# Performance work log

Measured on AMD Instinct MI355X. Metric: run time of the kernel, lower is better.

Reference implementation:

```python
import jax, jax.numpy as jnp
import numpy as np

B, T, D = 2, 4096, 512
H, W = 8, 32
HD = D // H            # 64
HIDDEN = 3 * D         # SwiGLU expansion = 3
SCALE = float(np.sqrt(HD))
EPS = 1e-5


def setup_inputs() -> dict:
    key = jax.random.key(0)
    ks = jax.random.split(key, 8)
    s = 0.02  # small init for weight matrices
    return {
        "x": jax.random.normal(ks[0], (B, T, D), dtype=jnp.float32),
        "pre_g": jnp.ones((D,), jnp.float32), "pre_b": jnp.zeros((D,), jnp.float32),
        "wq": jax.random.normal(ks[1], (D, D), jnp.float32) * s,
        "wkv": jax.random.normal(ks[2], (D, 2 * D), jnp.float32) * s,
        "wo": jax.random.normal(ks[3], (D, D), jnp.float32) * s,
        "attn_g": jnp.ones((D,), jnp.float32), "attn_b": jnp.zeros((D,), jnp.float32),
        "freqs": jax.random.normal(ks[4], (D,), jnp.float32) * 0.02,
        "phases": jnp.zeros((D,), jnp.float32),
        "amp": jnp.full((1,), 0.1, jnp.float32),
        "w_gate": jax.random.normal(ks[5], (D, HIDDEN), jnp.float32) * s,
        "w_val": jax.random.normal(ks[6], (D, HIDDEN), jnp.float32) * s,
        "w_proj": jax.random.normal(ks[7], (HIDDEN, D), jnp.float32) * s,
        "ffn_g": jnp.ones((D,), jnp.float32), "ffn_b": jnp.zeros((D,), jnp.float32),
    }


def _ln(x, g, b):
    mu = jnp.mean(x, axis=-1, keepdims=True)
    var = jnp.mean(jnp.square(x - mu), axis=-1, keepdims=True)
    return (x - mu) * jax.lax.rsqrt(var + EPS) * g + b


def _gather_window(z):
    # z: (B, T, H, C) -> nb: (B, T, W, H, C) with nb[:, t, w] = z[:, t-1-w] (zeros if t-1-w < 0)
    zp = jnp.pad(z, ((0, 0), (W, 0), (0, 0), (0, 0)))
    idx = jnp.arange(T)[:, None] + (W - 1) - jnp.arange(W)[None, :]  # (T, W), values in [0, T+W-1)
    return zp[:, idx]  # (B, T, W, H, C)


def reference(x, pre_g, pre_b, wq, wkv, wo, attn_g, attn_b,
              freqs, phases, amp, w_gate, w_val, w_proj, ffn_g, ffn_b):
    h = _ln(x, pre_g, pre_b)

    # ---- multi-head causal tension (sigmoid local attention) ----
    q = (h @ wq).reshape(B, T, H, HD)
    kv = (h @ wkv).reshape(B, T, H, 2 * HD)
    nb_kv = _gather_window(kv)                     # (B, T, W, H, 2*HD)
    nb_k, nb_v = nb_kv[..., :HD], nb_kv[..., HD:]
    tau = jax.nn.sigmoid(jnp.einsum('bthd,btwhd->bthw', q, nb_k) / SCALE)
    msg = jnp.einsum('bthw,btwhd->bthd', tau, nb_v).reshape(B, T, D)
    h = _ln(h + msg @ wo, attn_g, attn_b)

    # ---- oscillatory modulation ----
    pos = jnp.arange(T, dtype=jnp.float32)[:, None]  # (T, 1)
    mod = jnp.sin(pos * freqs + phases)              # (T, D)
    y = h * (1.0 + amp * mod)[None]

    # ---- SwiGLU FFN ----
    z = (jax.nn.silu(y @ w_gate) * (y @ w_val)) @ w_proj
    return _ln(y + z, ffn_g, ffn_b)
```

## Files before the change

### kernel.cpp

```cpp
#include <hip/hip_runtime.h>
#include <hip/hip_bf16.h>
#include <math.h>

#define T_LEN   4096
#define D_DIM   512
#define H_NUM   8
#define HD_DIM  64
#define W_WIN   32
#define HID_DIM 1536
#define M_ROWS  8192
#define QKV_LD  1536
#define BK 64

typedef __hip_bfloat16 bf16;
typedef __bf16  bf16x8 __attribute__((ext_vector_type(8)));
typedef float   f32x4  __attribute__((ext_vector_type(4)));

#define G_AS __attribute__((address_space(1)))
#define L_AS __attribute__((address_space(3)))

__device__ __forceinline__ float b2f(bf16 x) { return __bfloat162float(x); }
__device__ __forceinline__ bf16  f2b(float x){ return __float2bfloat16(x); }

__device__ __forceinline__ void gload_lds16(const bf16* g, bf16* l) {
  __builtin_amdgcn_global_load_lds((const G_AS unsigned int*)g,
                                   (L_AS unsigned int*)l, 16, 0, 0);
}

__device__ __forceinline__ float rdP(const void* p, int i, bool f32) {
  return f32 ? ((const float*)p)[i] : b2f(((const bf16*)p)[i]);
}

__device__ __forceinline__ float wave_reduce_sum(float v) {
  #pragma unroll
  for (int off = 32; off; off >>= 1) v += __shfl_xor(v, off, 64);
  return v;
}

__device__ __forceinline__ bool detect_f32(const unsigned* __restrict__ x) {
  int lane = threadIdx.x & 63;
  int votes = 0;
  #pragma unroll
  for (int i = 0; i < 4; ++i) {
    unsigned e = (x[lane * 4 + i] >> 7) & 0xffu;
    votes += (e >= 90u && e <= 140u) ? 1 : 0;
  }
  float v = wave_reduce_sum((float)votes);
  return v < 200.f;
}

__device__ __forceinline__ void swizzle_xy(int gx, int& bx, int& by) {
  int lid = blockIdx.x;
  int sub = lid & 7;
  int grp = lid >> 3;
  bx = grp % gx;
  by = (grp / gx) * 8 + sub;
}

__global__ __launch_bounds__(256) void ln_kernel(
    const void* __restrict__ in, const void* __restrict__ g, const void* __restrict__ bb,
    void* __restrict__ out, int mode,
    const void* __restrict__ freqs, const void* __restrict__ phases,
    const void* __restrict__ amp,
    const unsigned* __restrict__ xdet, int in_follows, int out_follows)
{
  bool f32  = detect_f32(xdet);
  bool inF  = f32 && (in_follows != 0);
  bool outF = f32 && (out_follows != 0);

  int wave = threadIdx.x >> 6;
  int lane = threadIdx.x & 63;
  int row  = blockIdx.x * 4 + wave;

  float x[8];
  if (inF) {
    const float* rp = (const float*)in + (size_t)row * D_DIM + lane * 8;
    float4 v0 = *reinterpret_cast<const float4*>(rp);
    float4 v1 = *reinterpret_cast<const float4*>(rp + 4);
    x[0]=v0.x; x[1]=v0.y; x[2]=v0.z; x[3]=v0.w;
    x[4]=v1.x; x[5]=v1.y; x[6]=v1.z; x[7]=v1.w;
  } else {
    bf16x8 v = *reinterpret_cast<const bf16x8*>(
        (const bf16*)in + (size_t)row * D_DIM + lane * 8);
    #pragma unroll
    for (int i = 0; i < 8; ++i) x[i] = (float)v[i];
  }

  float s = 0.f, s2 = 0.f;
  #pragma unroll
  for (int i = 0; i < 8; ++i) { s += x[i]; s2 += x[i]*x[i]; }
  s  = wave_reduce_sum(s);
  s2 = wave_reduce_sum(s2);
  float mu   = s * (1.f / D_DIM);
  float var  = s2 * (1.f / D_DIM) - mu * mu;
  float rstd = rsqrtf(var + 1e-5f);

  int t = row & (T_LEN - 1);
  float ampf = (mode == 1) ? rdP(amp, 0, f32) : 0.f;

  float o[8];
  #pragma unroll
  for (int i = 0; i < 8; ++i) {
    int d = lane * 8 + i;
    float val = (x[i] - mu) * rstd * rdP(g, d, f32) + rdP(bb, d, f32);
    if (mode == 1) {
      float m = sinf(fmaf((float)t, rdP(freqs, d, f32), rdP(phases, d, f32)));
      val *= (1.f + ampf * m);
    }
    o[i] = val;
  }

  if (outF) {
    float* op = (float*)out + (size_t)row * D_DIM + lane * 8;
    *reinterpret_cast<float4*>(op)     = make_float4(o[0], o[1], o[2], o[3]);
    *reinterpret_cast<float4*>(op + 4) = make_float4(o[4], o[5], o[6], o[7]);
  } else {
    bf16x8 ov;
    #pragma unroll
    for (int i = 0; i < 8; ++i) ov[i] = (__bf16)o[i];
    *reinterpret_cast<bf16x8*>((bf16*)out + (size_t)row * D_DIM + lane * 8) = ov;
  }
}

__global__ __launch_bounds__(256) void transpose_all_kernel(
    const void* s0, const void* s1, const void* s2, const void* s3,
    const void* s4, const void* s5,
    bf16* d0, bf16* d1, bf16* d2, bf16* d3, bf16* d4, bf16* d5,
    const unsigned* __restrict__ xdet)
{
  bool f32 = detect_f32(xdet);
  int bid = blockIdx.x;
  const void* src; bf16* dst; int R, C, lid, tiles_x;
  if      (bid < 256)  { src=s0; dst=d0; R=512;  C=512;  lid=bid;      tiles_x=16; }
  else if (bid < 768)  { src=s1; dst=d1; R=512;  C=1024; lid=bid-256;  tiles_x=32; }
  else if (bid < 1024) { src=s2; dst=d2; R=512;  C=512;  lid=bid-768;  tiles_x=16; }
  else if (bid < 1792) { src=s3; dst=d3; R=512;  C=1536; lid=bid-1024; tiles_x=48; }
  else if (bid < 2560) { src=s4; dst=d4; R=512;  C=1536; lid=bid-1792; tiles_x=48; }
  else                 { src=s5; dst=d5; R=1536; C=512;  lid=bid-2560; tiles_x=16; }

  __shared__ bf16 tile[32][33];
  int tx = threadIdx.x & 31;
  int ty = threadIdx.x >> 5;
  int c0 = (lid % tiles_x) * 32;
  int r0 = (lid / tiles_x) * 32;
  #pragma unroll
  for (int j = 0; j < 32; j += 8)
    tile[ty + j][tx] = f2b(rdP(src, (size_t)(r0 + ty + j) * C + c0 + tx, f32));
  __syncthreads();
  #pragma unroll
  for (int j = 0; j < 32; j += 8)
    dst[(size_t)(c0 + ty + j) * R + r0 + tx] = tile[tx][ty + j];
}

template<int BNT>
__global__ __launch_bounds__(256) void gemm_tile_kernel(
    const bf16* __restrict__ A, const bf16* __restrict__ Bt,
    bf16* Cout, const bf16* extra, int N, int K, int lda, int mode, int gx)
{
  constexpr int BJ = BNT / 32;
  __shared__ alignas(16) bf16 As[128 * BK];
  __shared__ alignas(16) bf16 Bs[BNT * BK];

  int bx, by; swizzle_xy(gx, bx, by);
  int mbase = by * 128, nbase = bx * BNT;
  int tid  = threadIdx.x;
  int lane = tid & 63;
  int wid  = tid >> 6;
  int quad = lane >> 4, l16 = lane & 15;
  int wm = (wid >> 1) * 64, wn = (wid & 1) * (BNT / 2);

  int srow = tid >> 3;
  int scol = (tid & 7) ^ (srow & 7);
  const bf16* Ag = A  + (size_t)(mbase + srow) * lda + scol * 8;
  const bf16* Bg = Bt + (size_t)(nbase + srow) * K   + scol * 8;

  f32x4 acc[4][BJ] = {};

  for (int kleft = K / BK; kleft > 0; --kleft) {
    __syncthreads();
    #pragma unroll
    for (int j = 0; j < 4; ++j)
      gload_lds16(Ag + (size_t)(j * 32) * lda, &As[j * 2048 + tid * 8]);
    #pragma unroll
    for (int j = 0; j < BJ; ++j)
      gload_lds16(Bg + (size_t)(j * 32) * K,   &Bs[j * 2048 + tid * 8]);
    Ag += BK; Bg += BK;
    __syncthreads();

    #pragma unroll
    for (int ko = 0; ko < 2; ++ko) {
      bf16x8 a[4], b[BJ];
      int c = ((ko * 4 + quad) ^ (l16 & 7)) * 8;
      #pragma unroll
      for (int i = 0; i < 4; ++i)
        a[i] = *reinterpret_cast<const bf16x8*>(&As[(wm + i * 16 + l16) * BK + c]);
      #pragma unroll
      for (int j = 0; j < BJ; ++j)
        b[j] = *reinterpret_cast<const bf16x8*>(&Bs[(wn + j * 16 + l16) * BK + c]);
      #pragma unroll
      for (int i = 0; i < 4; ++i)
        #pragma unroll
        for (int j = 0; j < BJ; ++j)
          acc[i][j] = __builtin_amdgcn_mfma_f32_16x16x32_bf16(a[i], b[j], acc[i][j], 0, 0, 0);
    }
  }

  #pragma unroll
  for (int i = 0; i < 4; ++i)
    #pragma unroll
    for (int j = 0; j < BJ; ++j)
      #pragma unroll
      for (int r = 0; r < 4; ++r) {
        int row = mbase + wm + i * 16 + quad * 4 + r;
        int col = nbase + wn + j * 16 + l16;
        size_t idx = (size_t)row * N + col;
        float cv = acc[i][j][r];
        if (mode == 1) cv += b2f(extra[idx]);
        Cout[idx] = f2b(cv);
      }
}

__global__ __launch_bounds__(256) void gateval_kernel(
    const bf16* __restrict__ A, const bf16* __restrict__ Btg,
    const bf16* __restrict__ Btv, bf16* __restrict__ Cout,
    int N, int K, int lda, int gx)
{
  __shared__ alignas(16) bf16 As [128 * BK];
  __shared__ alignas(16) bf16 Bgs[ 64 * BK];
  __shared__ alignas(16) bf16 Bvs[ 64 * BK];

  int bx, by; swizzle_xy(gx, bx, by);
  int mbase = by * 128, nbase = bx * 64;
  int tid  = threadIdx.x;
  int lane = tid & 63;
  int wid  = tid >> 6;
  int quad = lane >> 4, l16 = lane & 15;
  int wm = (wid >> 1) * 64, wn = (wid & 1) * 32;

  int srow = tid >> 3;
  int scol = (tid & 7) ^ (srow & 7);
  const bf16* Ag = A   + (size_t)(mbase + srow) * lda + scol * 8;
  const bf16* Gg = Btg + (size_t)(nbase + srow) * K   + scol * 8;
  const bf16* Vg = Btv + (size_t)(nbase + srow) * K   + scol * 8;

  f32x4 accg[4][2] = {};
  f32x4 accv[4][2] = {};

  for (int kleft = K / BK; kleft > 0; --kleft) {
    __syncthreads();
    #pragma unroll
    for (int j = 0; j < 4; ++j)
      gload_lds16(Ag + (size_t)(j * 32) * lda, &As[j * 2048 + tid * 8]);
    #pragma unroll
    for (int j = 0; j < 2; ++j) {
      gload_lds16(Gg + (size_t)(j * 32) * K, &Bgs[j * 2048 + tid * 8]);
      gload_lds16(Vg + (size_t)(j * 32) * K, &Bvs[j * 2048 + tid * 8]);
    }
    Ag += BK; Gg += BK; Vg += BK;
    __syncthreads();

    #pragma unroll
    for (int ko = 0; ko < 2; ++ko) {
      bf16x8 a[4], bg[2], bv[2];
      int c = ((ko * 4 + quad) ^ (l16 & 7)) * 8;
      #pragma unroll
      for (int i = 0; i < 4; ++i)
        a[i]  = *reinterpret_cast<const bf16x8*>(&As [(wm + i * 16 + l16) * BK + c]);
      #pragma unroll
      for (int j = 0; j < 2; ++j) {
        bg[j] = *reinterpret_cast<const bf16x8*>(&Bgs[(wn + j * 16 + l16) * BK + c]);
        bv[j] = *reinterpret_cast<const bf16x8*>(&Bvs[(wn + j * 16 + l16) * BK + c]);
      }
      #pragma unroll
      for (int i = 0; i < 4; ++i)
        #pragma unroll
        for (int j = 0; j < 2; ++j) {
          accg[i][j] = __builtin_amdgcn_mfma_f32_16x16x32_bf16(a[i], bg[j], accg[i][j], 0, 0, 0);
          accv[i][j] = __builtin_amdgcn_mfma_f32_16x16x32_bf16(a[i], bv[j], accv[i][j], 0, 0, 0);
        }
    }
  }

  #pragma unroll
  for (int i = 0; i < 4; ++i)
    #pragma unroll
    for (int j = 0; j < 2; ++j)
      #pragma unroll
      for (int r = 0; r < 4; ++r) {
        int row = mbase + wm + i * 16 + quad * 4 + r;
        int col = nbase + wn + j * 16 + l16;
        float g = accg[i][j][r];
        float v = accv[i][j][r];
        Cout[(size_t)row * N + col] = f2b(g / (1.f + expf(-g)) * v);
      }
}

#define VT_BYTES 9216
#define PL_BYTES 2304
#define ATTN_SET (VT_BYTES + PL_BYTES)
__device__ __forceinline__ int vt_addr(int d, int t) { return d * 144 + t * 2; }

__global__ __launch_bounds__(256) void attn_mfma_kernel(bf16* qkv)
{
  __shared__ alignas(16) char lds_raw[4 * ATTN_SET];
  int lane = threadIdx.x & 63;
  int widx = threadIdx.x >> 6;
  int u    = blockIdx.x * 4 + widx;
  int tile = u >> 3, head = u & 7;
  int rowbase = tile * 16;
  int t0   = rowbase & (T_LEN - 1);
  int l16  = lane & 15, quad = lane >> 4;

  char* wbase = lds_raw + widx * ATTN_SET;
  char* Vl = wbase;
  bf16* Pl = (bf16*)(wbase + VT_BYTES);

  #pragma unroll
  for (int it = 0; it < 6; ++it) {
    int chunk = it * 64 + lane;
    int t  = chunk >> 3;
    int dc = chunk & 7;
    int row = rowbase - 32 + t;
    if (row < 0) row = 0;
    bf16x8 v = *reinterpret_cast<const bf16x8*>(
        qkv + (size_t)row * QKV_LD + 512 + head * 128 + 64 + dc * 8);
    #pragma unroll
    for (int jj = 0; jj < 8; ++jj)
      *(bf16*)(Vl + vt_addr(dc * 8 + jj, t)) = (bf16)(__bf16)v[jj];
  }
  bf16x8 z = {};
  *reinterpret_cast<bf16x8*>(Vl + vt_addr(lane, 48)) = z;
  *reinterpret_cast<bf16x8*>(Vl + vt_addr(lane, 56)) = z;

  bf16x8 aq0, aq1;
  {
    const bf16* qrow = qkv + (size_t)(rowbase + l16) * QKV_LD + head * HD_DIM + quad * 8;
    aq0 = *reinterpret_cast<const bf16x8*>(qrow);
    aq1 = *reinterpret_cast<const bf16x8*>(qrow + 32);
  }

  f32x4 sacc[3] = {};
  #pragma unroll
  for (int jt = 0; jt < 3; ++jt) {
    int tok = rowbase - 32 + jt * 16 + l16;
    if (tok < 0) tok = 0;
    const bf16* krow = qkv + (size_t)tok * QKV_LD + 512 + head * 128 + quad * 8;
    bf16x8 b0 = *reinterpret_cast<const bf16x8*>(krow);
    bf16x8 b1 = *reinterpret_cast<const bf16x8*>(krow + 32);
    sacc[jt] = __builtin_amdgcn_mfma_f32_16x16x32_bf16(aq0, b0, sacc[jt], 0, 0, 0);
    sacc[jt] = __builtin_amdgcn_mfma_f32_16x16x32_bf16(aq1, b1, sacc[jt], 0, 0, 0);
  }

  #pragma unroll
  for (int jt = 0; jt < 3; ++jt) {
    int j = jt * 16 + l16;
    #pragma unroll
    for (int r = 0; r < 4; ++r) {
      int i = quad * 4 + r;
      bool valid = (j >= i) && (j <= i + 31) && (t0 - 32 + j >= 0);
      float tau = valid ? 1.f / (1.f + expf(-sacc[jt][r] * 0.125f)) : 0.f;
      Pl[i * 72 + j] = f2b(tau);
    }
  }
  #pragma unroll
  for (int r = 0; r < 4; ++r) Pl[(quad * 4 + r) * 72 + 48 + l16] = f2b(0.f);

  __syncthreads();

  bf16x8 ap0 = *reinterpret_cast<const bf16x8*>((char*)Pl + l16 * 144 + quad * 16);
  bf16x8 ap1 = *reinterpret_cast<const bf16x8*>((char*)Pl + l16 * 144 + 64 + quad * 16);

  f32x4 macc[4] = {};
  #pragma unroll
  for (int nt = 0; nt < 4; ++nt) {
    int d = nt * 16 + l16;
    bf16x8 bv0 = *reinterpret_cast<const bf16x8*>(Vl + vt_addr(d, quad * 8));
    bf16x8 bv1 = *reinterpret_cast<const bf16x8*>(Vl + vt_addr(d, 32 + quad * 8));
    macc[nt] = __builtin_amdgcn_mfma_f32_16x16x32_bf16(ap0, bv0, macc[nt], 0, 0, 0);
    macc[nt] = __builtin_amdgcn_mfma_f32_16x16x32_bf16(ap1, bv1, macc[nt], 0, 0, 0);
  }

  #pragma unroll
  for (int nt = 0; nt < 4; ++nt)
    #pragma unroll
    for (int r = 0; r < 4; ++r)
      qkv[(size_t)(rowbase + quad * 4 + r) * QKV_LD + head * HD_DIM + nt * 16 + l16] =
          f2b(macc[nt][r]);
}

extern "C" void kernel_launch(void* const* d_in, const int* in_sizes, int n_in,
                              void* d_out, int out_size, void* d_ws, size_t ws_size,
                              hipStream_t stream)
{
  const void* x      = d_in[0];
  const void* pre_g  = d_in[1];
  const void* pre_b  = d_in[2];
  const void* wq     = d_in[3];
  const void* wkv    = d_in[4];
  const void* wo     = d_in[5];
  const void* attn_g = d_in[6];
  const void* attn_b = d_in[7];
  const void* freqs  = d_in[8];
  const void* phases = d_in[9];
  const void* amp    = d_in[10];
  const void* w_gate = d_in[11];
  const void* w_val  = d_in[12];
  const void* w_proj = d_in[13];
  const void* ffn_g  = d_in[14];
  const void* ffn_b  = d_in[15];
  const unsigned* xdet = (const unsigned*)x;

  char* ws = (char*)d_ws;
  bf16* Btqkv = (bf16*)(ws + 512);
  bf16* Bto   = (bf16*)(ws + 1573376);
  bf16* Btg   = (bf16*)(ws + 2097664);
  bf16* Btv   = (bf16*)(ws + 3670528);
  bf16* Btp   = (bf16*)(ws + 5243392);
  bf16* h     = (bf16*)(ws + 6816256);
  bf16* qkvb  = (bf16*)(ws + 15204864);
  bf16* gb    = qkvb;

  transpose_all_kernel<<<3328, 256, 0, stream>>>(
      wq, wkv, wo, w_gate, w_val, w_proj,
      Btqkv, Btqkv + 512 * 512, Bto, Btg, Btv, Btp, xdet);

  ln_kernel<<<2048, 256, 0, stream>>>(x, pre_g, pre_b, h, 0,
                                      nullptr, nullptr, nullptr, xdet, 1, 0);

  gemm_tile_kernel<128><<<768, 256, 0, stream>>>(h, Btqkv, qkvb, nullptr,
                                                 1536, 512, 512, 0, 12);

  attn_mfma_kernel<<<1024, 256, 0, stream>>>(qkvb);

  gemm_tile_kernel<64><<<512, 256, 0, stream>>>(qkvb, Bto, h, h,
                                                512, 512, QKV_LD, 1, 8);

  ln_kernel<<<2048, 256, 0, stream>>>(h, attn_g, attn_b, h, 1,
                                      freqs, phases, amp, xdet, 0, 0);

  gateval_kernel<<<1536, 256, 0, stream>>>(h, Btg, Btv, gb,
                                           1536, 512, 512, 24);

  gemm_tile_kernel<64><<<512, 256, 0, stream>>>(gb, Btp, h, h,
                                                512, 1536, QKV_LD, 1, 8);

  ln_kernel<<<2048, 256, 0, stream>>>(h, ffn_g, ffn_b, d_out, 0,
                                      nullptr, nullptr, nullptr, xdet, 0, 1);
}
```

Before: 298.9 us.

## Double-buffer LDS tiles in GEMM kernels to overlap global loads with MFMA

```diff
diff --git a/kernel.cpp b/kernel.cpp
--- a/kernel.cpp
+++ b/kernel.cpp
@@ -18,6 +18,11 @@
 
 #define G_AS __attribute__((address_space(1)))
 #define L_AS __attribute__((address_space(3)))
+
+#define SBAR()        __builtin_amdgcn_s_barrier()
+#define SCHED_FENCE() __builtin_amdgcn_sched_barrier(0)
+#define WAIT_VM(N)    asm volatile("s_waitcnt vmcnt(" #N ")" ::: "memory")
+#define WAIT_LGKM0()  asm volatile("s_waitcnt lgkmcnt(0)" ::: "memory")
 
 __device__ __forceinline__ float b2f(bf16 x) { return __bfloat162float(x); }
 __device__ __forceinline__ bf16  f2b(float x){ return __float2bfloat16(x); }
@@ -158,8 +163,8 @@
     bf16* Cout, const bf16* extra, int N, int K, int lda, int mode, int gx)
 {
   constexpr int BJ = BNT / 32;
-  __shared__ alignas(16) bf16 As[128 * BK];
-  __shared__ alignas(16) bf16 Bs[BNT * BK];
+  __shared__ alignas(16) bf16 As[2][128 * BK];
+  __shared__ alignas(16) bf16 Bs[2][BNT * BK];
 
   int bx, by; swizzle_xy(gx, bx, by);
   int mbase = by * 128, nbase = bx * BNT;
@@ -175,17 +180,33 @@
   const bf16* Bg = Bt + (size_t)(nbase + srow) * K   + scol * 8;
 
   f32x4 acc[4][BJ] = {};
-
-  for (int kleft = K / BK; kleft > 0; --kleft) {
-    __syncthreads();
-    #pragma unroll
-    for (int j = 0; j < 4; ++j)
-      gload_lds16(Ag + (size_t)(j * 32) * lda, &As[j * 2048 + tid * 8]);
-    #pragma unroll
-    for (int j = 0; j < BJ; ++j)
-      gload_lds16(Bg + (size_t)(j * 32) * K,   &Bs[j * 2048 + tid * 8]);
-    Ag += BK; Bg += BK;
-    __syncthreads();
+  int nk = K / BK;
+
+  #pragma unroll
+  for (int j = 0; j < 4; ++j)
+    gload_lds16(Ag + (size_t)(j * 32) * lda, &As[0][j * 2048 + tid * 8]);
+  #pragma unroll
+  for (int j = 0; j < BJ; ++j)
+    gload_lds16(Bg + (size_t)(j * 32) * K,   &Bs[0][j * 2048 + tid * 8]);
+  Ag += BK; Bg += BK;
+
+  for (int t = 0; t < nk; ++t) {
+    int cur = t & 1;
+    if (t + 1 < nk) {
+      int nxt = cur ^ 1;
+      #pragma unroll
+      for (int j = 0; j < 4; ++j)
+        gload_lds16(Ag + (size_t)(j * 32) * lda, &As[nxt][j * 2048 + tid * 8]);
+      #pragma unroll
+      for (int j = 0; j < BJ; ++j)
+        gload_lds16(Bg + (size_t)(j * 32) * K,   &Bs[nxt][j * 2048 + tid * 8]);
+      Ag += BK; Bg += BK;
+      if constexpr (BNT == 128) { WAIT_VM(8); } else { WAIT_VM(6); }
+    } else {
+      WAIT_VM(0);
+    }
+    SBAR();
+    SCHED_FENCE();
 
     #pragma unroll
     for (int ko = 0; ko < 2; ++ko) {
@@ -193,16 +214,20 @@
       int c = ((ko * 4 + quad) ^ (l16 & 7)) * 8;
       #pragma unroll
       for (int i = 0; i < 4; ++i)
-        a[i] = *reinterpret_cast<const bf16x8*>(&As[(wm + i * 16 + l16) * BK + c]);
+        a[i] = *reinterpret_cast<const bf16x8*>(&As[cur][(wm + i * 16 + l16) * BK + c]);
       #pragma unroll
       for (int j = 0; j < BJ; ++j)
-        b[j] = *reinterpret_cast<const bf16x8*>(&Bs[(wn + j * 16 + l16) * BK + c]);
+        b[j] = *reinterpret_cast<const bf16x8*>(&Bs[cur][(wn + j * 16 + l16) * BK + c]);
       #pragma unroll
       for (int i = 0; i < 4; ++i)
         #pragma unroll
         for (int j = 0; j < BJ; ++j)
           acc[i][j] = __builtin_amdgcn_mfma_f32_16x16x32_bf16(a[i], b[j], acc[i][j], 0, 0, 0);
     }
+
+    WAIT_LGKM0();
+    SBAR();
+    SCHED_FENCE();
   }
 
   #pragma unroll
@@ -225,9 +250,9 @@
     const bf16* __restrict__ Btv, bf16* __restrict__ Cout,
     int N, int K, int lda, int gx)
 {
-  __shared__ alignas(16) bf16 As [128 * BK];
-  __shared__ alignas(16) bf16 Bgs[ 64 * BK];
-  __shared__ alignas(16) bf16 Bvs[ 64 * BK];
+  __shared__ alignas(16) bf16 As [2][128 * BK];
+  __shared__ alignas(16) bf16 Bgs[2][ 64 * BK];
+  __shared__ alignas(16) bf16 Bvs[2][ 64 * BK];
 
   int bx, by; swizzle_xy(gx, bx, by);
   int mbase = by * 128, nbase = bx * 64;
@@ -245,19 +270,37 @@
 
   f32x4 accg[4][2] = {};
   f32x4 accv[4][2] = {};
-
-  for (int kleft = K / BK; kleft > 0; --kleft) {
-    __syncthreads();
-    #pragma unroll
-    for (int j = 0; j < 4; ++j)
-      gload_lds16(Ag + (size_t)(j * 32) * lda, &As[j * 2048 + tid * 8]);
-    #pragma unroll
-    for (int j = 0; j < 2; ++j) {
-      gload_lds16(Gg + (size_t)(j * 32) * K, &Bgs[j * 2048 + tid * 8]);
-      gload_lds16(Vg + (size_t)(j * 32) * K, &Bvs[j * 2048 + tid * 8]);
-    }
-    Ag += BK; Gg += BK; Vg += BK;
-    __syncthreads();
+  int nk = K / BK;
+
+  #pragma unroll
+  for (int j = 0; j < 4; ++j)
+    gload_lds16(Ag + (size_t)(j * 32) * lda, &As[0][j * 2048 + tid * 8]);
+  #pragma unroll
+  for (int j = 0; j < 2; ++j) {
+    gload_lds16(Gg + (size_t)(j * 32) * K, &Bgs[0][j * 2048 + tid * 8]);
+    gload_lds16(Vg + (size_t)(j * 32) * K, &Bvs[0][j * 2048 + tid * 8]);
+  }
+  Ag += BK; Gg += BK; Vg += BK;
+
+  for (int t = 0; t < nk; ++t) {
+    int cur = t & 1;
+    if (t + 1 < nk) {
+      int nxt = cur ^ 1;
+      #pragma unroll
+      for (int j = 0; j < 4; ++j)
+        gload_lds16(Ag + (size_t)(j * 32) * lda, &As[nxt][j * 2048 + tid * 8]);
+      #pragma unroll
+      for (int j = 0; j < 2; ++j) {
+        gload_lds16(Gg + (size_t)(j * 32) * K, &Bgs[nxt][j * 2048 + tid * 8]);
+        gload_lds16(Vg + (size_t)(j * 32) * K, &Bvs[nxt][j * 2048 + tid * 8]);
+      }
+      Ag += BK; Gg += BK; Vg += BK;
+      WAIT_VM(8);
+    } else {
+      WAIT_VM(0);
+    }
+    SBAR();
+    SCHED_FENCE();
 
     #pragma unroll
     for (int ko = 0; ko < 2; ++ko) {
@@ -265,11 +308,11 @@
       int c = ((ko * 4 + quad) ^ (l16 & 7)) * 8;
       #pragma unroll
       for (int i = 0; i < 4; ++i)
-        a[i]  = *reinterpret_cast<const bf16x8*>(&As [(wm + i * 16 + l16) * BK + c]);
+        a[i]  = *reinterpret_cast<const bf16x8*>(&As [cur][(wm + i * 16 + l16) * BK + c]);
       #pragma unroll
       for (int j = 0; j < 2; ++j) {
-        bg[j] = *reinterpret_cast<const bf16x8*>(&Bgs[(wn + j * 16 + l16) * BK + c]);
-        bv[j] = *reinterpret_cast<const bf16x8*>(&Bvs[(wn + j * 16 + l16) * BK + c]);
+        bg[j] = *reinterpret_cast<const bf16x8*>(&Bgs[cur][(wn + j * 16 + l16) * BK + c]);
+        bv[j] = *reinterpret_cast<const bf16x8*>(&Bvs[cur][(wn + j * 16 + l16) * BK + c]);
       }
       #pragma unroll
       for (int i = 0; i < 4; ++i)
@@ -279,6 +322,10 @@
           accv[i][j] = __builtin_amdgcn_mfma_f32_16x16x32_bf16(a[i], bv[j], accv[i][j], 0, 0, 0);
         }
     }
+
+    WAIT_LGKM0();
+    SBAR();
+    SCHED_FENCE();
   }
 
   #pragma unroll
```

Result: no change. 297.7 us (-0.4%).
